# Performance work log

Measured on AMD Instinct MI355X. Metric: run time of the kernel, lower is better.

Reference implementation:

```python
import jax, jax.numpy as jnp
import numpy as np

H = 768        # hidden_size (rubert-base)
WDIM = 30      # width_embedding_dim (SpanRepresentation default)
MAXW = 10      # max_span_width
HID = 150      # PairwiseScorer hidden_dim
LN_EPS = 1e-5


def setup_inputs() -> dict:
    key = jax.random.key(0)
    ks = jax.random.split(key, 12)
    B, S, N = 4, 2048, 4096
    p = lambda i, shape: jax.random.normal(ks[i], shape, dtype=jnp.float32) * 0.02
    return {
        "sequence_output": jax.random.normal(ks[0], (B, S, H), dtype=jnp.float32),
        "span_starts": jax.random.randint(ks[1], (B, N), 0, S),
        "span_ends": jax.random.randint(ks[2], (B, N), 0, S),
        "W_start": p(3, (H, H)), "b_start": jnp.zeros((H,), jnp.float32),
        "W_end": p(4, (H, H)), "b_end": jnp.zeros((H,), jnp.float32),
        "width_emb": p(5, (MAXW + 1, WDIM)),
        "W_out": p(6, (2 * H + WDIM, H)), "b_out": jnp.zeros((H,), jnp.float32),
        "w_ment": p(7, (H,)), "b_ment": jnp.zeros((), jnp.float32),
        "W1": p(8, (4 * H, HID)), "b1": jnp.zeros((HID,), jnp.float32),
        "ln_g": jnp.ones((HID,), jnp.float32), "ln_b": jnp.zeros((HID,), jnp.float32),
        "W2": p(9, (HID,)), "b2": jnp.zeros((), jnp.float32),
        "top_k": 128,
    }


def reference(sequence_output, span_starts, span_ends,
              W_start, b_start, W_end, b_end, width_emb, W_out, b_out,
              w_ment, b_ment, W1, b1, ln_g, ln_b, W2, b2, top_k):
    # --- SpanRepresentation: gather endpoints, endpoint FFs, width embedding ---
    st = jnp.take_along_axis(sequence_output, span_starts[..., None], axis=1)  # [B,N,H]
    en = jnp.take_along_axis(sequence_output, span_ends[..., None], axis=1)    # [B,N,H]
    start_e = st @ W_start + b_start
    end_e = en @ W_end + b_end
    widths = jnp.clip(span_ends - span_starts, 0, MAXW)
    we = width_emb[widths]                                                     # [B,N,WDIM]
    span_repr = jnp.concatenate([start_e, end_e, we], axis=-1) @ W_out + b_out # [B,N,H]

    # --- MentionScorer + top-k filtering (per batch, vectorized) ---
    scores = span_repr @ w_ment + b_ment                                       # [B,N]
    mention_scores, idx = jax.lax.top_k(scores, top_k)                         # [B,K]
    repr_k = jnp.take_along_axis(span_repr, idx[..., None], axis=1)            # [B,K,H]
    f_starts = jnp.take_along_axis(span_starts, idx, axis=1)
    f_ends = jnp.take_along_axis(span_ends, idx, axis=1)

    # --- PairwiseScorer over all pairs: cat([s1,s2,s1-s2,s1*s2]) @ W1 ---
    # Split W1 rows into the four feature blocks; fold the (s1-s2) block in:
    #   z = s1@(Wa+Wc) + s2@(Wb-Wc) + (s1*s2)@Wd + b1
    Wa, Wb, Wc, Wd = W1[:H], W1[H:2*H], W1[2*H:3*H], W1[3*H:]
    u = repr_k @ (Wa + Wc)                                                     # [B,K,HID]
    v = repr_k @ (Wb - Wc)                                                     # [B,K,HID]
    pw = jnp.einsum('bih,bjh,hd->bijd', repr_k, repr_k, Wd)                    # [B,K,K,HID]
    z = u[:, :, None, :] + v[:, None, :, :] + pw + b1
    h = jax.nn.relu(z)
    mu = jnp.mean(h, axis=-1, keepdims=True)
    var = jnp.mean(jnp.square(h - mu), axis=-1, keepdims=True)
    hn = (h - mu) * jax.lax.rsqrt(var + LN_EPS) * ln_g + ln_b
    # Dropout(0.3) is identity in eval mode.
    ant = hn @ W2 + b2                                                         # [B,K,K]
    ant = jnp.tril(ant, k=-1)

    return (mention_scores, ant, f_starts, f_ends)
```

## Files before the change

kernel.cpp:

```cpp
#include <hip/hip_runtime.h>
#include <math.h>

#define H 768
#define SEQ 2048
#define NSP 4096
#define HIDD 150
#define TOPK 128
#define NPAD 160

#define OFS_ANT 512
#define OFS_FS 66048
#define OFS_FE 66560

static const size_t OFF_T     = 0ull;
static const size_t OFF_BIASP = 8448ull;
static const size_t OFF_WOV   = 14592ull;
static const size_t OFF_AV    = 16128ull;
static const size_t OFF_CV    = 16896ull;
static const size_t OFF_TW    = 17664ull;
static const size_t OFF_PD    = 17680ull;
static const size_t OFF_CAND  = 34064ull;
static const size_t OFF_FS    = 42256ull;
static const size_t OFF_FE    = 42768ull;
static const size_t OFF_WID   = 43280ull;
static const size_t OFF_UVP   = 43792ull;
static const size_t OFF_GW    = 371472ull;
static const size_t OFF_SCAL  = 371632ull;
static const size_t OFF_WF    = 371640ull;
static const size_t OFF_WCF   = 433080ull;
static const size_t OFF_WSF   = 555960ull;
static const size_t OFF_WEF   = 850872ull;
static const size_t OFF_WOF   = 1145784ull;
static const size_t OFF_GSEH  = 1735608ull;
static const size_t OFF_SEH   = 2128824ull;
static const size_t OFF_RKH   = 2522040ull;
static const size_t OFF_RKP2  = 2718648ull;

typedef __attribute__((ext_vector_type(8))) _Float16 half8;
typedef __attribute__((ext_vector_type(4))) _Float16 half4;
typedef __attribute__((ext_vector_type(4))) float f32x4;

__global__ __launch_bounds__(256) void kA(
    const float* __restrict__ b_start, const float* __restrict__ b_end,
    const float* __restrict__ b_out, const float* __restrict__ W_out,
    const float* __restrict__ w_ment, const float* __restrict__ W1,
    const float* __restrict__ ln_g, const float* __restrict__ ln_b,
    const float* __restrict__ W2, const float* __restrict__ b2,
    const float* __restrict__ W_start, const float* __restrict__ W_end,
    float* __restrict__ biasP, float* __restrict__ WOV,
    _Float16* __restrict__ WF, _Float16* __restrict__ WCF,
    _Float16* __restrict__ WSF, _Float16* __restrict__ WEF,
    _Float16* __restrict__ WOF, float* __restrict__ GW, float* __restrict__ SCAL) {
    const int blk = blockIdx.x, tid = threadIdx.x;
    if (blk < 24) {
        const int kc = blk / 3, jb = blk - kc * 3;
        const int j = jb * 256 + tid;
        float acc = (kc == 0) ? b_out[j] : 0.f;
        const int k0 = kc * 96;
#pragma unroll 4
        for (int k = k0; k < k0 + 96; ++k) {
            acc += b_start[k] * W_out[(size_t)k * H + j];
            acc += b_end[k]   * W_out[(size_t)(H + k) * H + j];
        }
        biasP[kc * H + j] = acc;
    } else if (blk < 408) {
        const int wid = tid >> 6, lane = tid & 63;
        const int gr = (blk - 24) * 4 + wid;
        const float* row = W_out + (size_t)gr * H;
        float s = 0.f;
#pragma unroll
        for (int q = 0; q < 12; ++q) s += row[lane + 64 * q] * w_ment[lane + 64 * q];
#pragma unroll
        for (int off = 32; off; off >>= 1) s += __shfl_down(s, off, 64);
        if (lane == 0) WOV[gr] = s;
    } else if (blk < 468) {
        const int idx = (blk - 408) * 256 + tid;
        const int nt = idx / 1536;
        const int rem = idx - nt * 1536;
        const int kt = rem >> 6, lane = rem & 63;
        const int n = nt * 16 + (lane & 15);
        const int kb = kt * 32 + (lane >> 4) * 8;
        _Float16* dst = WF + (size_t)idx * 8;
#pragma unroll
        for (int e = 0; e < 8; ++e) {
            float v = (n < HIDD) ? W1[(size_t)(3 * H + kb + e) * HIDD + n] : 0.f;
            dst[e] = (_Float16)v;
        }
    } else if (blk < 588) {
        const int idx = (blk - 468) * 256 + tid;
        const int nt = idx / 1536;
        const int rem = idx - nt * 1536;
        const int kt = rem >> 6, lane = rem & 63;
        const int n = nt * 16 + (lane & 15);
        const int kb = kt * 32 + (lane >> 4) * 8;
        _Float16* dst = WCF + (size_t)idx * 8;
#pragma unroll
        for (int e = 0; e < 8; ++e) {
            const int h = kb + e;
            float v = 0.f;
            if (n < 160) {
                if (n < HIDD)
                    v = W1[(size_t)h * HIDD + n] + W1[(size_t)(2 * H + h) * HIDD + n];
            } else {
                const int d = n - 160;
                if (d < HIDD)
                    v = W1[(size_t)(H + h) * HIDD + d] - W1[(size_t)(2 * H + h) * HIDD + d];
            }
            dst[e] = (_Float16)v;
        }
    } else if (blk == 588) {
        if (tid < NPAD) GW[tid] = (tid < HIDD) ? ln_g[tid] * W2[tid] : 0.f;
        if (tid == 0) {
            float sg = 0.f, sb = 0.f;
            for (int d = 0; d < HIDD; ++d) { sg += ln_g[d] * W2[d]; sb += ln_b[d] * W2[d]; }
            SCAL[0] = sg;
            SCAL[1] = sb + b2[0];
        }
    } else if (blk < 1165) {
        const bool isS = blk < 877;
        const int idx = (blk - (isS ? 589 : 877)) * 256 + tid;
        const float* Wsrc = isS ? W_start : W_end;
        _Float16* dstb = isS ? WSF : WEF;
        const int nt = idx / 1536;
        const int rem = idx - nt * 1536;
        const int kt = rem >> 6, lane = rem & 63;
        const int n = nt * 16 + (lane & 15);
        const int kb = kt * 32 + (lane >> 4) * 8;
        _Float16* dst = dstb + (size_t)idx * 8;
#pragma unroll
        for (int e = 0; e < 8; ++e) dst[e] = (_Float16)Wsrc[(size_t)(kb + e) * H + n];
    } else {
        const int idx = (blk - 1165) * 256 + tid;
        const int nt = idx / 3072;
        const int rem = idx - nt * 3072;
        const int kt = rem >> 6, lane = rem & 63;
        const int n = nt * 16 + (lane & 15);
        const int kb = kt * 32 + (lane >> 4) * 8;
        _Float16* dst = WOF + (size_t)idx * 8;
#pragma unroll
        for (int e = 0; e < 8; ++e) dst[e] = (_Float16)W_out[(size_t)(kb + e) * H + n];
    }
}

__global__ __launch_bounds__(256) void kB(
    const float* __restrict__ biasP, const float* __restrict__ width_emb,
    const float* __restrict__ W_out, const float* __restrict__ W_start,
    const float* __restrict__ W_end, const float* __restrict__ WOV,
    float* __restrict__ T, float* __restrict__ av, float* __restrict__ cv) {
    const int blk = blockIdx.x, tid = threadIdx.x;
    if (blk < 33) {
        const int w = blk / 3, jb = blk - w * 3;
        const int j = jb * 256 + tid;
        float acc = 0.f;
#pragma unroll
        for (int kc = 0; kc < 8; ++kc) acc += biasP[kc * H + j];
#pragma unroll
        for (int k = 0; k < 30; ++k)
            acc += width_emb[w * 30 + k] * W_out[(size_t)(2 * H + k) * H + j];
        T[w * H + j] = acc;
    } else {
        const int wid = tid >> 6, lane = tid & 63;
        const int gr = (blk - 33) * 4 + wid;
        const float* row = (gr < H) ? (W_start + (size_t)gr * H) : (W_end + (size_t)(gr - H) * H);
        const float* vec = (gr < H) ? WOV : (WOV + H);
        float s = 0.f;
#pragma unroll
        for (int q = 0; q < 12; ++q) s += row[lane + 64 * q] * vec[lane + 64 * q];
#pragma unroll
        for (int off = 32; off; off >>= 1) s += __shfl_down(s, off, 64);
        if (lane == 0) {
            if (gr < H) av[gr] = s; else cv[gr - H] = s;
        }
    }
}

__global__ void k_posdots(const float* __restrict__ seq, const float* __restrict__ av,
                          const float* __restrict__ cv, const float* __restrict__ T,
                          const float* __restrict__ w_ment, const float* __restrict__ b_ment,
                          float* __restrict__ PD, float* __restrict__ tw) {
    const int wid = threadIdx.x >> 6, lane = threadIdx.x & 63;
    if (blockIdx.x < 2048) {
        const int r = blockIdx.x * 4 + wid;
        const float4* row = (const float4*)(seq + (size_t)r * H);
        const float4* a4 = (const float4*)av;
        const float4* c4 = (const float4*)cv;
        float sa = 0.f, sc = 0.f;
#pragma unroll
        for (int q = 0; q < 3; ++q) {
            float4 x = row[lane + 64 * q];
            float4 ya = a4[lane + 64 * q], yc = c4[lane + 64 * q];
            sa += x.x * ya.x + x.y * ya.y + x.z * ya.z + x.w * ya.w;
            sc += x.x * yc.x + x.y * yc.y + x.z * yc.z + x.w * yc.w;
        }
#pragma unroll
        for (int off = 32; off; off >>= 1) {
            sa += __shfl_down(sa, off, 64);
            sc += __shfl_down(sc, off, 64);
        }
        if (lane == 0) { PD[r] = sa; PD[8192 + r] = sc; }
    } else {
        for (int w = wid; w <= 10; w += 4) {
            float s = 0.f;
#pragma unroll
            for (int q = 0; q < 12; ++q) s += T[w * H + lane + 64 * q] * w_ment[lane + 64 * q];
#pragma unroll
            for (int off = 32; off; off >>= 1) s += __shfl_down(s, off, 64);
            if (lane == 0) tw[w] = s + b_ment[0];
        }
    }
}

__global__ __launch_bounds__(256) void k_sort1(const float* __restrict__ PD,
    const int* __restrict__ starts, const int* __restrict__ ends,
    const float* __restrict__ tw, unsigned long long* __restrict__ CAND) {
    __shared__ unsigned long long keys[512];
    const int blk = blockIdx.x;
    const int b = blk >> 3, c = blk & 7;
    const int tid = threadIdx.x;
    for (int i = tid; i < 512; i += 256) {
        const int gi = c * 512 + i;
        const int r = b * NSP + gi;
        const int s = starts[r], e = ends[r];
        int w = e - s; w = w < 0 ? 0 : (w > 10 ? 10 : w);
        const float sc = PD[b * SEQ + s] + PD[8192 + b * SEQ + e] + tw[w];
        unsigned u = __float_as_uint(sc);
        u = (u & 0x80000000u) ? ~u : (u | 0x80000000u);
        keys[i] = ((unsigned long long)u << 32) | (unsigned)(0xFFFFFFFFu - (unsigned)gi);
    }
    __syncthreads();
    for (int k = 2; k <= 512; k <<= 1) {
        for (int j = k >> 1; j > 0; j >>= 1) {
            const int p = tid;
            const int i = ((p & ~(j - 1)) << 1) | (p & (j - 1));
            const int l = i | j;
            unsigned long long a = keys[i], d = keys[l];
            const bool desc = ((i & k) == 0);
            if ((a < d) == desc) { keys[i] = d; keys[l] = a; }
            __syncthreads();
        }
    }
    if (tid < 128) CAND[(size_t)(b * 8 + c) * 128 + tid] = keys[tid];
}

__global__ __launch_bounds__(256) void k_sort2(const unsigned long long* __restrict__ CAND,
    const int* __restrict__ starts, const int* __restrict__ ends,
    float* __restrict__ out, int* __restrict__ fsI, int* __restrict__ feI,
    int* __restrict__ widI) {
    __shared__ unsigned long long K[1024];
    const int b = blockIdx.x, tid = threadIdx.x;
    for (int i = tid; i < 1024; i += 256) K[i] = CAND[(size_t)b * 1024 + i];
    __syncthreads();
    for (int nl = 4; nl >= 1; nl >>= 1) {
        const int items = nl * 128;
        unsigned long long v0 = 0, v1 = 0;
        if (tid < items) {
            const int q = tid >> 7, r = tid & 127;
            unsigned long long a = K[q * 256 + r];
            unsigned long long d = K[q * 256 + 128 + (127 - r)];
            v0 = a > d ? a : d;
        }
        if (tid + 256 < items) {
            const int i = tid + 256;
            const int q = i >> 7, r = i & 127;
            unsigned long long a = K[q * 256 + r];
            unsigned long long d = K[q * 256 + 128 + (127 - r)];
            v1 = a > d ? a : d;
        }
        __syncthreads();
        if (tid < items) K[(tid >> 7) * 128 + (tid & 127)] = v0;
        if (tid + 256 < items) { const int i = tid + 256; K[(i >> 7) * 128 + (i & 127)] = v1; }
        __syncthreads();
        for (int j = 64; j; j >>= 1) {
            const int pairs = nl * 64;
            for (int i = tid; i < pairs; i += 256) {
                const int q = i >> 6, r = i & 63;
                const int lo = q * 128 + (((r & ~(j - 1)) << 1) | (r & (j - 1)));
                const int hi = lo + j;
                unsigned long long a = K[lo], d = K[hi];
                if (a < d) { K[lo] = d; K[hi] = a; }
            }
            __syncthreads();
        }
    }
    if (tid < TOPK) {
        const unsigned long long key = K[tid];
        const int widx = (int)(0xFFFFFFFFu - (unsigned)(key & 0xFFFFFFFFu));
        const unsigned hu = (unsigned)(key >> 32);
        const float sval = __uint_as_float((hu & 0x80000000u) ? (hu & 0x7FFFFFFFu) : ~hu);
        const int s = starts[b * NSP + widx], e = ends[b * NSP + widx];
        const int p = b * TOPK + tid;
        out[p] = sval;
        out[OFS_FS + p] = (float)s;
        out[OFS_FE + p] = (float)e;
        fsI[p] = b * SEQ + s;
        feI[p] = b * SEQ + e;
        int w = e - s;
        widI[p] = w < 0 ? 0 : (w > 10 ? 10 : w);
    }
}

__global__ void k_gath(const float* __restrict__ seq, const int* __restrict__ fsI,
                       const int* __restrict__ feI, _Float16* __restrict__ GSEH) {
    const int r0 = blockIdx.x * 4;
    const int tid = threadIdx.x;
    for (int q = 0; q < 4; ++q) {
        const int row = r0 + q;
        const int src = (row < 512) ? fsI[row] : feI[row - 512];
        if (tid < 192) {
            float4 v = *(const float4*)(seq + (size_t)src * H + tid * 4);
            half4 h = {(_Float16)v.x, (_Float16)v.y, (_Float16)v.z, (_Float16)v.w};
            *(half4*)(GSEH + (size_t)row * H + tid * 4) = h;
        }
    }
}

__global__ __launch_bounds__(256) void k_gemm1(const _Float16* __restrict__ GSEH,
    const _Float16* __restrict__ WSF, const _Float16* __restrict__ WEF,
    _Float16* __restrict__ SEH) {
    const int mt = blockIdx.x;
    const int wave = threadIdx.x >> 6, lane = threadIdx.x & 63;
    const int nt0 = blockIdx.y * 8 + wave * 2;
    const _Float16* Arow = GSEH + (size_t)(mt * 16 + (lane & 15)) * H + (lane >> 4) * 8;
    const _Float16* BF = (mt < 32) ? WSF : WEF;
    f32x4 acc0 = {0.f, 0.f, 0.f, 0.f}, acc1 = acc0;
    for (int kt = 0; kt < 24; ++kt) {
        half8 a = *(const half8*)(Arow + kt * 32);
        half8 b0 = *(const half8*)(BF + ((size_t)((nt0 * 24 + kt) * 64 + lane)) * 8);
        half8 b1 = *(const half8*)(BF + ((size_t)(((nt0 + 1) * 24 + kt) * 64 + lane)) * 8);
        acc0 = __builtin_amdgcn_mfma_f32_16x16x32_f16(a, b0, acc0, 0, 0, 0);
        acc1 = __builtin_amdgcn_mfma_f32_16x16x32_f16(a, b1, acc1, 0, 0, 0);
    }
    const int c = lane & 15, quad = lane >> 4;
#pragma unroll
    for (int r = 0; r < 4; ++r) {
        const int row = mt * 16 + quad * 4 + r;
        SEH[(size_t)row * H + nt0 * 16 + c] = (_Float16)acc0[r];
        SEH[(size_t)row * H + (nt0 + 1) * 16 + c] = (_Float16)acc1[r];
    }
}

__global__ __launch_bounds__(256) void k_gemm2(const _Float16* __restrict__ SEH,
    const _Float16* __restrict__ WOF, float* __restrict__ RKP2) {
    const int mt = blockIdx.x, kh = blockIdx.z;
    const int wave = threadIdx.x >> 6, lane = threadIdx.x & 63;
    const int nt0 = blockIdx.y * 8 + wave * 2;
    const _Float16* Arow = SEH + (size_t)(kh * 512 + mt * 16 + (lane & 15)) * H + (lane >> 4) * 8;
    f32x4 acc0 = {0.f, 0.f, 0.f, 0.f}, acc1 = acc0;
    for (int kt2 = 0; kt2 < 24; ++kt2) {
        const int kt = kh * 24 + kt2;
        half8 a = *(const half8*)(Arow + kt2 * 32);
        half8 b0 = *(const half8*)(WOF + ((size_t)((nt0 * 48 + kt) * 64 + lane)) * 8);
        half8 b1 = *(const half8*)(WOF + ((size_t)(((nt0 + 1) * 48 + kt) * 64 + lane)) * 8);
        acc0 = __builtin_amdgcn_mfma_f32_16x16x32_f16(a, b0, acc0, 0, 0, 0);
        acc1 = __builtin_amdgcn_mfma_f32_16x16x32_f16(a, b1, acc1, 0, 0, 0);
    }
    const int c = lane & 15, quad = lane >> 4;
    float* dst = RKP2 + (size_t)kh * 512 * H;
#pragma unroll
    for (int r = 0; r < 4; ++r) {
        const int row = mt * 16 + quad * 4 + r;
        dst[(size_t)row * H + nt0 * 16 + c] = acc0[r];
        dst[(size_t)row * H + (nt0 + 1) * 16 + c] = acc1[r];
    }
}

__global__ void k_fin(const float* __restrict__ RKP2, const float* __restrict__ T,
                      const int* __restrict__ widI, _Float16* __restrict__ RKH) {
    const int p = blockIdx.x, tid = threadIdx.x;
    if (tid >= 192) return;
    const int w = widI[p];
    const int c0 = tid * 4;
    float4 s = *(const float4*)(T + (size_t)w * H + c0);
    float4 v0 = *(const float4*)(RKP2 + (size_t)p * H + c0);
    float4 v1 = *(const float4*)(RKP2 + (size_t)(512 + p) * H + c0);
    half4 h = {(_Float16)(s.x + v0.x + v1.x), (_Float16)(s.y + v0.y + v1.y),
               (_Float16)(s.z + v0.z + v1.z), (_Float16)(s.w + v0.w + v1.w)};
    *(half4*)(RKH + (size_t)p * H + c0) = h;
}

__global__ __launch_bounds__(256) void k_uv3(const _Float16* __restrict__ RKH,
    const _Float16* __restrict__ WCF, float* __restrict__ UVP) {
    const int t = blockIdx.x, kh = blockIdx.y;
    const int wave = threadIdx.x >> 6, lane = threadIdx.x & 63;
    const _Float16* Arow = RKH + (size_t)(t * 16 + (lane & 15)) * H + (lane >> 4) * 8;
    f32x4 acc[5];
#pragma unroll
    for (int q = 0; q < 5; ++q) acc[q] = (f32x4){0.f, 0.f, 0.f, 0.f};
    for (int kk = 0; kk < 12; ++kk) {
        const int kt = kh * 12 + kk;
        half8 a = *(const half8*)(Arow + kt * 32);
#pragma unroll
        for (int q = 0; q < 5; ++q) {
            const int nt = wave * 5 + q;
            half8 bv = *(const half8*)(WCF + ((size_t)((nt * 24 + kt) * 64 + lane)) * 8);
            acc[q] = __builtin_amdgcn_mfma_f32_16x16x32_f16(a, bv, acc[q], 0, 0, 0);
        }
    }
    const int c = lane & 15, g = lane >> 4;
#pragma unroll
    for (int q = 0; q < 5; ++q) {
        const int n = (wave * 5 + q) * 16 + c;
#pragma unroll
        for (int r = 0; r < 4; ++r) {
            const int p = t * 16 + g * 4 + r;
            UVP[((size_t)kh * 512 + p) * 320 + n] = acc[q][r];
        }
    }
}

__global__ __launch_bounds__(256) void k_pair(
    const _Float16* __restrict__ WF, const _Float16* __restrict__ RKH,
    const float* __restrict__ UVP, const float* __restrict__ b1,
    const float* __restrict__ GW, const float* __restrict__ SCAL,
    float* __restrict__ ant) {
    const int ii = blockIdx.x, b = blockIdx.y;
    float* arow = ant + ((size_t)b * TOPK + ii) * TOPK;
    const int tid = threadIdx.x;
    if (tid < TOPK && tid >= ii) arow[tid] = 0.f;
    const int ntiles = (ii + 15) >> 4;
    if (ntiles == 0) return;

    const int wave = tid >> 6, lane = tid & 63;
    const int g = lane >> 4, c = lane & 15;
    const int t0 = wave, t1 = wave + 4;
    const bool has0 = t0 < ntiles, has1 = t1 < ntiles;

    __shared__ _Float16 sB[2][5120];

    const _Float16* RiH = RKH + (size_t)(b * TOPK + ii) * H;
    const _Float16* Rj0 = RKH + (size_t)(b * TOPK + t0 * 16 + c) * H + g * 8;
    const _Float16* Rj1 = RKH + (size_t)(b * TOPK + t1 * 16 + c) * H + g * 8;

    f32x4 acc0[10], acc1[10];
#pragma unroll
    for (int nt = 0; nt < 10; ++nt) {
        acc0[nt] = (f32x4){0.f, 0.f, 0.f, 0.f};
        acc1[nt] = (f32x4){0.f, 0.f, 0.f, 0.f};
    }

    auto stage_src = [&](int kt, int i) -> uint4 {
        const int nt = i >> 6, wi = i & 63;
        return *(const uint4*)(WF + ((size_t)((nt * 24 + kt) * 64 + wi)) * 8);
    };

    uint4 s0 = stage_src(0, tid);
    uint4 s1 = stage_src(0, tid + 256);
    uint4 s2;
    if (tid < 128) s2 = stage_src(0, tid + 512);
    {
        uint4* sbw = (uint4*)sB[0];
        sbw[tid] = s0;
        sbw[tid + 256] = s1;
        if (tid < 128) sbw[tid + 512] = s2;
    }
    half8 rj0, rj1, ri;
    if (has0) rj0 = *(const half8*)(Rj0);
    if (has1) rj1 = *(const half8*)(Rj1);
    ri = *(const half8*)(RiH + g * 8);
    __syncthreads();

    for (int kt = 0; kt < 24; ++kt) {
        const int cur = kt & 1, nxt = cur ^ 1;
        uint4 n0, n1, n2;
        half8 nrj0, nrj1, nri;
        if (kt < 23) {
            n0 = stage_src(kt + 1, tid);
            n1 = stage_src(kt + 1, tid + 256);
            if (tid < 128) n2 = stage_src(kt + 1, tid + 512);
            if (has0) nrj0 = *(const half8*)(Rj0 + (kt + 1) * 32);
            if (has1) nrj1 = *(const half8*)(Rj1 + (kt + 1) * 32);
            nri = *(const half8*)(RiH + (kt + 1) * 32 + g * 8);
        }
        half8 a0, a1;
        if (has0) a0 = ri * rj0;
        if (has1) a1 = ri * rj1;
#pragma unroll
        for (int nt = 0; nt < 10; ++nt) {
            half8 bv = *(const half8*)&sB[cur][nt * 512 + lane * 8];
            if (has0) acc0[nt] = __builtin_amdgcn_mfma_f32_16x16x32_f16(a0, bv, acc0[nt], 0, 0, 0);
            if (has1) acc1[nt] = __builtin_amdgcn_mfma_f32_16x16x32_f16(a1, bv, acc1[nt], 0, 0, 0);
        }
        if (kt < 23) {
            uint4* sbw = (uint4*)sB[nxt];
            sbw[tid] = n0;
            sbw[tid + 256] = n1;
            if (tid < 128) sbw[tid + 512] = n2;
            rj0 = nrj0; rj1 = nrj1; ri = nri;
        }
        __syncthreads();
    }

    const float Sgw = SCAL[0], C0 = SCAL[1];
    const int pi = b * TOPK + ii;
    float u10[10], gw10[10];
#pragma unroll
    for (int nt = 0; nt < 10; ++nt) {
        const int d = nt * 16 + c;
        const float ub = (d < HIDD) ? b1[d] : 0.f;
        u10[nt] = UVP[(size_t)pi * 320 + d] + UVP[(size_t)(512 + pi) * 320 + d] + ub;
        gw10[nt] = GW[d];
    }
    auto epi = [&](const f32x4 (&acc)[10], int t) {
#pragma unroll
        for (int r = 0; r < 4; ++r) {
            const int j = 16 * t + g * 4 + r;
            const int pj = b * TOPK + j;
            const float* Vp0 = UVP + (size_t)pj * 320 + 160;
            const float* Vp1 = UVP + (size_t)(512 + pj) * 320 + 160;
            float s1 = 0.f, s2 = 0.f, s3 = 0.f;
#pragma unroll
            for (int nt = 0; nt < 10; ++nt) {
                const int d = nt * 16 + c;
                float z = acc[nt][r] + u10[nt] + Vp0[d] + Vp1[d];
                float h = (d < HIDD && z > 0.f) ? z : 0.f;
                s1 += h;
                s2 += h * h;
                s3 += h * gw10[nt];
            }
#pragma unroll
            for (int off = 1; off < 16; off <<= 1) {
                s1 += __shfl_xor(s1, off, 64);
                s2 += __shfl_xor(s2, off, 64);
                s3 += __shfl_xor(s3, off, 64);
            }
            const float mu = s1 * (1.f / HIDD);
            const float var = s2 * (1.f / HIDD) - mu * mu;
            const float rstd = rsqrtf(var + 1e-5f);
            const float val = rstd * (s3 - mu * Sgw) + C0;
            if (c == 0 && j < ii) arow[j] = val;
        }
    };
    if (has0) epi(acc0, t0);
    if (has1) epi(acc1, t1);
}

extern "C" void kernel_launch(void* const* d_in, const int* in_sizes, int n_in,
                              void* d_out, int out_size, void* d_ws, size_t ws_size,
                              hipStream_t stream) {
    const float* seq      = (const float*)d_in[0];
    const int*   starts   = (const int*)d_in[1];
    const int*   ends     = (const int*)d_in[2];
    const float* W_start  = (const float*)d_in[3];
    const float* b_start  = (const float*)d_in[4];
    const float* W_end    = (const float*)d_in[5];
    const float* b_end    = (const float*)d_in[6];
    const float* width_e  = (const float*)d_in[7];
    const float* W_out    = (const float*)d_in[8];
    const float* b_out    = (const float*)d_in[9];
    const float* w_ment   = (const float*)d_in[10];
    const float* b_ment   = (const float*)d_in[11];
    const float* W1       = (const float*)d_in[12];
    const float* b1       = (const float*)d_in[13];
    const float* ln_g     = (const float*)d_in[14];
    const float* ln_b     = (const float*)d_in[15];
    const float* W2       = (const float*)d_in[16];
    const float* b2       = (const float*)d_in[17];
    float* out = (float*)d_out;
    float* ws  = (float*)d_ws;

    float* Tt    = ws + OFF_T;
    float* biasP = ws + OFF_BIASP;
    float* WOV   = ws + OFF_WOV;
    float* av    = ws + OFF_AV;
    float* cv    = ws + OFF_CV;
    float* tw    = ws + OFF_TW;
    float* PD    = ws + OFF_PD;
    unsigned long long* CANDp = (unsigned long long*)(ws + OFF_CAND);
    int*   fsI   = (int*)(ws + OFF_FS);
    int*   feI   = (int*)(ws + OFF_FE);
    int*   widI  = (int*)(ws + OFF_WID);
    float* UVPp  = ws + OFF_UVP;
    float* GWp   = ws + OFF_GW;
    float* SCALp = ws + OFF_SCAL;
    _Float16* WFp   = (_Float16*)(ws + OFF_WF);
    _Float16* WCFp  = (_Float16*)(ws + OFF_WCF);
    _Float16* WSFp  = (_Float16*)(ws + OFF_WSF);
    _Float16* WEFp  = (_Float16*)(ws + OFF_WEF);
    _Float16* WOFp  = (_Float16*)(ws + OFF_WOF);
    _Float16* GSEHp = (_Float16*)(ws + OFF_GSEH);
    _Float16* SEHp  = (_Float16*)(ws + OFF_SEH);
    _Float16* RKHp  = (_Float16*)(ws + OFF_RKH);
    float* RKP2p = ws + OFF_RKP2;

    kA<<<1741, 256, 0, stream>>>(b_start, b_end, b_out, W_out, w_ment, W1,
                                 ln_g, ln_b, W2, b2, W_start, W_end,
                                 biasP, WOV, WFp, WCFp, WSFp, WEFp, WOFp, GWp, SCALp);
    kB<<<417, 256, 0, stream>>>(biasP, width_e, W_out, W_start, W_end, WOV, Tt, av, cv);
    k_posdots<<<2049, 256, 0, stream>>>(seq, av, cv, Tt, w_ment, b_ment, PD, tw);
    k_sort1<<<32, 256, 0, stream>>>(PD, starts, ends, tw, CANDp);
    k_sort2<<<4, 256, 0, stream>>>(CANDp, starts, ends, out, fsI, feI, widI);
    k_gath<<<256, 256, 0, stream>>>(seq, fsI, feI, GSEHp);
    k_gemm1<<<dim3(64, 6), 256, 0, stream>>>(GSEHp, WSFp, WEFp, SEHp);
    k_gemm2<<<dim3(32, 6, 2), 256, 0, stream>>>(SEHp, WOFp, RKP2p);
    k_fin<<<512, 192, 0, stream>>>(RKP2p, Tt, widI, RKHp);
    k_uv3<<<dim3(32, 2), 256, 0, stream>>>(RKHp, WCFp, UVPp);
    k_pair<<<dim3(128, 4), 256, 0, stream>>>(WFp, RKHp, UVPp, b1, GWp, SCALp,
                                             out + OFS_ANT);
}
```

Baseline: 210.3 us.

## Fuse gather into gemm1, fold finalize into gemm2, retile pairwise kernel over triangle

Removes the separate gather and finalize kernels. gemm1 now reads fp32 sequence rows directly and converts them to half, and gemm2 does the full K=1536 reduction and adds the width/bias table before writing half output. The pairwise kernel is remapped to a triangular grid of 8x16 (i,j) tiles that read W1 fragments, now stored in a kt-major layout, straight from global memory instead of staging them through shared memory. Zeroing of the antecedent output moves into the prep kernel. This cuts launches and intermediate traffic, at the cost of less parallelism in gemm2 and more global loads in the pair kernel.

```diff
diff --git a/kernel.cpp b/kernel.cpp
--- a/kernel.cpp
+++ b/kernel.cpp
@@ -31,10 +31,8 @@
 static const size_t OFF_WSF   = 555960ull;
 static const size_t OFF_WEF   = 850872ull;
 static const size_t OFF_WOF   = 1145784ull;
-static const size_t OFF_GSEH  = 1735608ull;
-static const size_t OFF_SEH   = 2128824ull;
-static const size_t OFF_RKH   = 2522040ull;
-static const size_t OFF_RKP2  = 2718648ull;
+static const size_t OFF_SEH   = 1735608ull;
+static const size_t OFF_RKH   = 2128824ull;
 
 typedef __attribute__((ext_vector_type(8))) _Float16 half8;
 typedef __attribute__((ext_vector_type(4))) _Float16 half4;
@@ -50,7 +48,8 @@
     float* __restrict__ biasP, float* __restrict__ WOV,
     _Float16* __restrict__ WF, _Float16* __restrict__ WCF,
     _Float16* __restrict__ WSF, _Float16* __restrict__ WEF,
-    _Float16* __restrict__ WOF, float* __restrict__ GW, float* __restrict__ SCAL) {
+    _Float16* __restrict__ WOF, float* __restrict__ GW, float* __restrict__ SCAL,
+    float* __restrict__ ant) {
     const int blk = blockIdx.x, tid = threadIdx.x;
     if (blk < 24) {
         const int kc = blk / 3, jb = blk - kc * 3;
@@ -80,7 +79,7 @@
         const int kt = rem >> 6, lane = rem & 63;
         const int n = nt * 16 + (lane & 15);
         const int kb = kt * 32 + (lane >> 4) * 8;
-        _Float16* dst = WF + (size_t)idx * 8;
+        _Float16* dst = WF + ((size_t)((kt * 10 + nt) * 64 + lane)) * 8;
 #pragma unroll
         for (int e = 0; e < 8; ++e) {
             float v = (n < HIDD) ? W1[(size_t)(3 * H + kb + e) * HIDD + n] : 0.f;
@@ -129,7 +128,7 @@
         _Float16* dst = dstb + (size_t)idx * 8;
 #pragma unroll
         for (int e = 0; e < 8; ++e) dst[e] = (_Float16)Wsrc[(size_t)(kb + e) * H + n];
-    } else {
+    } else if (blk < 1741) {
         const int idx = (blk - 1165) * 256 + tid;
         const int nt = idx / 3072;
         const int rem = idx - nt * 3072;
@@ -139,6 +138,9 @@
         _Float16* dst = WOF + (size_t)idx * 8;
 #pragma unroll
         for (int e = 0; e < 8; ++e) dst[e] = (_Float16)W_out[(size_t)(kb + e) * H + n];
+    } else {
+        const int idx = (blk - 1741) * 256 + tid;
+        *(float4*)(ant + (size_t)idx * 4) = make_float4(0.f, 0.f, 0.f, 0.f);
     }
 }
 
@@ -299,32 +301,24 @@
     }
 }
 
-__global__ void k_gath(const float* __restrict__ seq, const int* __restrict__ fsI,
-                       const int* __restrict__ feI, _Float16* __restrict__ GSEH) {
-    const int r0 = blockIdx.x * 4;
-    const int tid = threadIdx.x;
-    for (int q = 0; q < 4; ++q) {
-        const int row = r0 + q;
-        const int src = (row < 512) ? fsI[row] : feI[row - 512];
-        if (tid < 192) {
-            float4 v = *(const float4*)(seq + (size_t)src * H + tid * 4);
-            half4 h = {(_Float16)v.x, (_Float16)v.y, (_Float16)v.z, (_Float16)v.w};
-            *(half4*)(GSEH + (size_t)row * H + tid * 4) = h;
-        }
-    }
-}
-
-__global__ __launch_bounds__(256) void k_gemm1(const _Float16* __restrict__ GSEH,
+__global__ __launch_bounds__(256) void k_gemm1(const float* __restrict__ seq,
+    const int* __restrict__ fsI, const int* __restrict__ feI,
     const _Float16* __restrict__ WSF, const _Float16* __restrict__ WEF,
     _Float16* __restrict__ SEH) {
     const int mt = blockIdx.x;
     const int wave = threadIdx.x >> 6, lane = threadIdx.x & 63;
+    const int g = lane >> 4;
     const int nt0 = blockIdx.y * 8 + wave * 2;
-    const _Float16* Arow = GSEH + (size_t)(mt * 16 + (lane & 15)) * H + (lane >> 4) * 8;
+    const int gi = mt * 16 + (lane & 15);
+    const int src = (mt < 32) ? fsI[gi] : feI[gi - 512];
+    const float* Arow = seq + (size_t)src * H + g * 8;
     const _Float16* BF = (mt < 32) ? WSF : WEF;
     f32x4 acc0 = {0.f, 0.f, 0.f, 0.f}, acc1 = acc0;
     for (int kt = 0; kt < 24; ++kt) {
-        half8 a = *(const half8*)(Arow + kt * 32);
+        float4 v0 = *(const float4*)(Arow + kt * 32);
+        float4 v1 = *(const float4*)(Arow + kt * 32 + 4);
+        half8 a = {(_Float16)v0.x, (_Float16)v0.y, (_Float16)v0.z, (_Float16)v0.w,
+                   (_Float16)v1.x, (_Float16)v1.y, (_Float16)v1.z, (_Float16)v1.w};
         half8 b0 = *(const half8*)(BF + ((size_t)((nt0 * 24 + kt) * 64 + lane)) * 8);
         half8 b1 = *(const half8*)(BF + ((size_t)(((nt0 + 1) * 24 + kt) * 64 + lane)) * 8);
         acc0 = __builtin_amdgcn_mfma_f32_16x16x32_f16(a, b0, acc0, 0, 0, 0);
@@ -340,42 +334,30 @@
 }
 
 __global__ __launch_bounds__(256) void k_gemm2(const _Float16* __restrict__ SEH,
-    const _Float16* __restrict__ WOF, float* __restrict__ RKP2) {
-    const int mt = blockIdx.x, kh = blockIdx.z;
+    const _Float16* __restrict__ WOF, const float* __restrict__ T,
+    const int* __restrict__ widI, _Float16* __restrict__ RKH) {
+    const int mt = blockIdx.x;
     const int wave = threadIdx.x >> 6, lane = threadIdx.x & 63;
     const int nt0 = blockIdx.y * 8 + wave * 2;
-    const _Float16* Arow = SEH + (size_t)(kh * 512 + mt * 16 + (lane & 15)) * H + (lane >> 4) * 8;
+    const _Float16* A0 = SEH + (size_t)(mt * 16 + (lane & 15)) * H + (lane >> 4) * 8;
+    const _Float16* A1 = SEH + (size_t)(512 + mt * 16 + (lane & 15)) * H + (lane >> 4) * 8;
     f32x4 acc0 = {0.f, 0.f, 0.f, 0.f}, acc1 = acc0;
-    for (int kt2 = 0; kt2 < 24; ++kt2) {
-        const int kt = kh * 24 + kt2;
-        half8 a = *(const half8*)(Arow + kt2 * 32);
+    for (int kt = 0; kt < 48; ++kt) {
+        half8 a = (kt < 24) ? *(const half8*)(A0 + kt * 32)
+                            : *(const half8*)(A1 + (kt - 24) * 32);
         half8 b0 = *(const half8*)(WOF + ((size_t)((nt0 * 48 + kt) * 64 + lane)) * 8);
         half8 b1 = *(const half8*)(WOF + ((size_t)(((nt0 + 1) * 48 + kt) * 64 + lane)) * 8);
         acc0 = __builtin_amdgcn_mfma_f32_16x16x32_f16(a, b0, acc0, 0, 0, 0);
         acc1 = __builtin_amdgcn_mfma_f32_16x16x32_f16(a, b1, acc1, 0, 0, 0);
     }
     const int c = lane & 15, quad = lane >> 4;
-    float* dst = RKP2 + (size_t)kh * 512 * H;
 #pragma unroll
     for (int r = 0; r < 4; ++r) {
         const int row = mt * 16 + quad * 4 + r;
-        dst[(size_t)row * H + nt0 * 16 + c] = acc0[r];
-        dst[(size_t)row * H + (nt0 + 1) * 16 + c] = acc1[r];
-    }
-}
-
-__global__ void k_fin(const float* __restrict__ RKP2, const float* __restrict__ T,
-                      const int* __restrict__ widI, _Float16* __restrict__ RKH) {
-    const int p = blockIdx.x, tid = threadIdx.x;
-    if (tid >= 192) return;
-    const int w = widI[p];
-    const int c0 = tid * 4;
-    float4 s = *(const float4*)(T + (size_t)w * H + c0);
-    float4 v0 = *(const float4*)(RKP2 + (size_t)p * H + c0);
-    float4 v1 = *(const float4*)(RKP2 + (size_t)(512 + p) * H + c0);
-    half4 h = {(_Float16)(s.x + v0.x + v1.x), (_Float16)(s.y + v0.y + v1.y),
-               (_Float16)(s.z + v0.z + v1.z), (_Float16)(s.w + v0.w + v1.w)};
-    *(half4*)(RKH + (size_t)p * H + c0) = h;
+        const float* Tr = T + (size_t)widI[row] * H;
+        RKH[(size_t)row * H + nt0 * 16 + c] = (_Float16)(acc0[r] + Tr[nt0 * 16 + c]);
+        RKH[(size_t)row * H + (nt0 + 1) * 16 + c] = (_Float16)(acc1[r] + Tr[(nt0 + 1) * 16 + c]);
+    }
 }
 
 __global__ __launch_bounds__(256) void k_uv3(const _Float16* __restrict__ RKH,
@@ -413,23 +395,18 @@
     const float* __restrict__ UVP, const float* __restrict__ b1,
     const float* __restrict__ GW, const float* __restrict__ SCAL,
     float* __restrict__ ant) {
-    const int ii = blockIdx.x, b = blockIdx.y;
-    float* arow = ant + ((size_t)b * TOPK + ii) * TOPK;
-    const int tid = threadIdx.x;
-    if (tid < TOPK && tid >= ii) arow[tid] = 0.f;
-    const int ntiles = (ii + 15) >> 4;
-    if (ntiles == 0) return;
-
-    const int wave = tid >> 6, lane = tid & 63;
+    const int b = blockIdx.y;
+    int ti = 0, rem = blockIdx.x;
+    while (rem >= (ti >> 1) + 1) { rem -= (ti >> 1) + 1; ++ti; }
+    const int tj = rem;
+    const int wave = threadIdx.x >> 6, lane = threadIdx.x & 63;
     const int g = lane >> 4, c = lane & 15;
-    const int t0 = wave, t1 = wave + 4;
-    const bool has0 = t0 < ntiles, has1 = t1 < ntiles;
-
-    __shared__ _Float16 sB[2][5120];
-
-    const _Float16* RiH = RKH + (size_t)(b * TOPK + ii) * H;
-    const _Float16* Rj0 = RKH + (size_t)(b * TOPK + t0 * 16 + c) * H + g * 8;
-    const _Float16* Rj1 = RKH + (size_t)(b * TOPK + t1 * 16 + c) * H + g * 8;
+    const int i0 = ti * 8 + wave * 2;
+    const int j0 = tj * 16;
+
+    const _Float16* Ri0 = RKH + (size_t)(b * TOPK + i0) * H + g * 8;
+    const _Float16* Ri1 = RKH + (size_t)(b * TOPK + i0 + 1) * H + g * 8;
+    const _Float16* Rj  = RKH + (size_t)(b * TOPK + j0 + c) * H + g * 8;
 
     f32x4 acc0[10], acc1[10];
 #pragma unroll
@@ -438,72 +415,43 @@
         acc1[nt] = (f32x4){0.f, 0.f, 0.f, 0.f};
     }
 
-    auto stage_src = [&](int kt, int i) -> uint4 {
-        const int nt = i >> 6, wi = i & 63;
-        return *(const uint4*)(WF + ((size_t)((nt * 24 + kt) * 64 + wi)) * 8);
-    };
-
-    uint4 s0 = stage_src(0, tid);
-    uint4 s1 = stage_src(0, tid + 256);
-    uint4 s2;
-    if (tid < 128) s2 = stage_src(0, tid + 512);
-    {
-        uint4* sbw = (uint4*)sB[0];
-        sbw[tid] = s0;
-        sbw[tid + 256] = s1;
-        if (tid < 128) sbw[tid + 512] = s2;
-    }
-    half8 rj0, rj1, ri;
-    if (has0) rj0 = *(const half8*)(Rj0);
-    if (has1) rj1 = *(const half8*)(Rj1);
-    ri = *(const half8*)(RiH + g * 8);
-    __syncthreads();
-
     for (int kt = 0; kt < 24; ++kt) {
-        const int cur = kt & 1, nxt = cur ^ 1;
-        uint4 n0, n1, n2;
-        half8 nrj0, nrj1, nri;
-        if (kt < 23) {
-            n0 = stage_src(kt + 1, tid);
-            n1 = stage_src(kt + 1, tid + 256);
-            if (tid < 128) n2 = stage_src(kt + 1, tid + 512);
-            if (has0) nrj0 = *(const half8*)(Rj0 + (kt + 1) * 32);
-            if (has1) nrj1 = *(const half8*)(Rj1 + (kt + 1) * 32);
-            nri = *(const half8*)(RiH + (kt + 1) * 32 + g * 8);
-        }
-        half8 a0, a1;
-        if (has0) a0 = ri * rj0;
-        if (has1) a1 = ri * rj1;
+        half8 bv[10];
+        const _Float16* wsrc = WF + (size_t)kt * 5120 + (size_t)lane * 8;
+#pragma unroll
+        for (int nt = 0; nt < 10; ++nt) bv[nt] = *(const half8*)(wsrc + nt * 512);
+        half8 rj  = *(const half8*)(Rj + kt * 32);
+        half8 ri0 = *(const half8*)(Ri0 + kt * 32);
+        half8 ri1 = *(const half8*)(Ri1 + kt * 32);
+        half8 a0 = ri0 * rj;
+        half8 a1 = ri1 * rj;
 #pragma unroll
         for (int nt = 0; nt < 10; ++nt) {
-            half8 bv = *(const half8*)&sB[cur][nt * 512 + lane * 8];
-            if (has0) acc0[nt] = __builtin_amdgcn_mfma_f32_16x16x32_f16(a0, bv, acc0[nt], 0, 0, 0);
-            if (has1) acc1[nt] = __builtin_amdgcn_mfma_f32_16x16x32_f16(a1, bv, acc1[nt], 0, 0, 0);
-        }
-        if (kt < 23) {
-            uint4* sbw = (uint4*)sB[nxt];
-            sbw[tid] = n0;
-            sbw[tid + 256] = n1;
-            if (tid < 128) sbw[tid + 512] = n2;
-            rj0 = nrj0; rj1 = nrj1; ri = nri;
-        }
-        __syncthreads();
+            acc0[nt] = __builtin_amdgcn_mfma_f32_16x16x32_f16(a0, bv[nt], acc0[nt], 0, 0, 0);
+            acc1[nt] = __builtin_amdgcn_mfma_f32_16x16x32_f16(a1, bv[nt], acc1[nt], 0, 0, 0);
+        }
     }
 
     const float Sgw = SCAL[0], C0 = SCAL[1];
-    const int pi = b * TOPK + ii;
-    float u10[10], gw10[10];
-#pragma unroll
-    for (int nt = 0; nt < 10; ++nt) {
-        const int d = nt * 16 + c;
-        const float ub = (d < HIDD) ? b1[d] : 0.f;
-        u10[nt] = UVP[(size_t)pi * 320 + d] + UVP[(size_t)(512 + pi) * 320 + d] + ub;
-        gw10[nt] = GW[d];
-    }
-    auto epi = [&](const f32x4 (&acc)[10], int t) {
+    float gw10[10];
+#pragma unroll
+    for (int nt = 0; nt < 10; ++nt) gw10[nt] = GW[nt * 16 + c];
+
+#pragma unroll
+    for (int iw = 0; iw < 2; ++iw) {
+        const int i = i0 + iw;
+        const int pi = b * TOPK + i;
+        float u10[10];
+#pragma unroll
+        for (int nt = 0; nt < 10; ++nt) {
+            const int d = nt * 16 + c;
+            const float ub = (d < HIDD) ? b1[d] : 0.f;
+            u10[nt] = UVP[(size_t)pi * 320 + d] + UVP[(size_t)(512 + pi) * 320 + d] + ub;
+        }
+        const f32x4* acc = iw ? acc1 : acc0;
 #pragma unroll
         for (int r = 0; r < 4; ++r) {
-            const int j = 16 * t + g * 4 + r;
+            const int j = j0 + g * 4 + r;
             const int pj = b * TOPK + j;
             const float* Vp0 = UVP + (size_t)pj * 320 + 160;
             const float* Vp1 = UVP + (size_t)(512 + pj) * 320 + 160;
@@ -527,11 +475,9 @@
             const float var = s2 * (1.f / HIDD) - mu * mu;
             const float rstd = rsqrtf(var + 1e-5f);
             const float val = rstd * (s3 - mu * Sgw) + C0;
-            if (c == 0 && j < ii) arow[j] = val;
-        }
-    };
-    if (has0) epi(acc0, t0);
-    if (has1) epi(acc1, t1);
+            if (c == 0 && j < i) ant[((size_t)b * TOPK + i) * TOPK + j] = val;
+        }
+    }
 }
 
 extern "C" void kernel_launch(void* const* d_in, const int* in_sizes, int n_in,
@@ -577,23 +523,20 @@
     _Float16* WSFp  = (_Float16*)(ws + OFF_WSF);
     _Float16* WEFp  = (_Float16*)(ws + OFF_WEF);
     _Float16* WOFp  = (_Float16*)(ws + OFF_WOF);
-    _Float16* GSEHp = (_Float16*)(ws + OFF_GSEH);
     _Float16* SEHp  = (_Float16*)(ws + OFF_SEH);
     _Float16* RKHp  = (_Float16*)(ws + OFF_RKH);
-    float* RKP2p = ws + OFF_RKP2;
-
-    kA<<<1741, 256, 0, stream>>>(b_start, b_end, b_out, W_out, w_ment, W1,
+
+    kA<<<1805, 256, 0, stream>>>(b_start, b_end, b_out, W_out, w_ment, W1,
                                  ln_g, ln_b, W2, b2, W_start, W_end,
-                                 biasP, WOV, WFp, WCFp, WSFp, WEFp, WOFp, GWp, SCALp);
+                                 biasP, WOV, WFp, WCFp, WSFp, WEFp, WOFp, GWp, SCALp,
+                                 out + OFS_ANT);
     kB<<<417, 256, 0, stream>>>(biasP, width_e, W_out, W_start, W_end, WOV, Tt, av, cv);
     k_posdots<<<2049, 256, 0, stream>>>(seq, av, cv, Tt, w_ment, b_ment, PD, tw);
     k_sort1<<<32, 256, 0, stream>>>(PD, starts, ends, tw, CANDp);
     k_sort2<<<4, 256, 0, stream>>>(CANDp, starts, ends, out, fsI, feI, widI);
-    k_gath<<<256, 256, 0, stream>>>(seq, fsI, feI, GSEHp);
-    k_gemm1<<<dim3(64, 6), 256, 0, stream>>>(GSEHp, WSFp, WEFp, SEHp);
-    k_gemm2<<<dim3(32, 6, 2), 256, 0, stream>>>(SEHp, WOFp, RKP2p);
-    k_fin<<<512, 192, 0, stream>>>(RKP2p, Tt, widI, RKHp);
+    k_gemm1<<<dim3(64, 6), 256, 0, stream>>>(seq, fsI, feI, WSFp, WEFp, SEHp);
+    k_gemm2<<<dim3(32, 6), 256, 0, stream>>>(SEHp, WOFp, Tt, widI, RKHp);
     k_uv3<<<dim3(32, 2), 256, 0, stream>>>(RKHp, WCFp, UVPp);
-    k_pair<<<dim3(128, 4), 256, 0, stream>>>(WFp, RKHp, UVPp, b1, GWp, SCALp,
-                                             out + OFS_ANT);
-}
+    k_pair<<<dim3(72, 4), 256, 0, stream>>>(WFp, RKHp, UVPp, b1, GWp, SCALp,
+                                            out + OFS_ANT);
+}
```

After: 228.4 us. 1.09x slower.
